# Performance work log

Hardware: AMD Instinct MI355X
Metric: run time of the kernel (lower is better)

The kernel has to match this reference:

```python
import jax, jax.numpy as jnp
import numpy as np


def setup_inputs() -> dict:
    key = jax.random.key(0)
    ks = jax.random.split(key, 8)
    T, D = 8192, 36
    return {
        "embeddings": jax.random.normal(ks[0], (T, D), dtype=jnp.float32),
        "WQ_prog": jax.random.normal(ks[1], (2, D), dtype=jnp.float32),
        "WK_prog": jax.random.normal(ks[2], (2, D), dtype=jnp.float32),
        "WV_op": jax.random.normal(ks[3], (1, D), dtype=jnp.float32),
        "WV_arg": jax.random.normal(ks[4], (1, D), dtype=jnp.float32),
        "WQ_stack": jax.random.normal(ks[5], (2, D), dtype=jnp.float32),
        "WK_stack": jax.random.normal(ks[6], (2, D), dtype=jnp.float32),
        "WV_stack": jax.random.normal(ks[7], (1, D), dtype=jnp.float32),
    }


def reference(embeddings, WQ_prog, WK_prog, WV_op, WV_arg, WQ_stack, WK_stack, WV_stack):
    # --- program-fetch head: hard-argmax attention ---
    Q_prog = embeddings @ WQ_prog.T          # (T, 2)
    K_prog = embeddings @ WK_prog.T          # (T, 2)
    V_op = embeddings @ WV_op.T              # (T, 1)
    V_arg = embeddings @ WV_arg.T            # (T, 1)
    scores_prog = Q_prog @ K_prog.T          # (T, T)
    best_prog = jnp.argmax(scores_prog, axis=1)   # (T,)
    fetched_ops = V_op[best_prog, 0]
    fetched_args = V_arg[best_prog, 0]

    # --- stack-fetch head: hard-argmax attention ---
    Q_stack = embeddings @ WQ_stack.T        # (T, 2)
    K_stack = embeddings @ WK_stack.T        # (T, 2)
    V_stack = embeddings @ WV_stack.T        # (T, 1)
    scores_stack = Q_stack @ K_stack.T       # (T, T)
    best_stack = jnp.argmax(scores_stack, axis=1)
    fetched_vals = V_stack[best_stack, 0]

    return (fetched_ops, fetched_args, fetched_vals)
```

## Files before the change

### kernel.cpp

```cpp
#include <hip/hip_runtime.h>
#include <math.h>

#define T 8192
#define D 36
#define NCH 64
#define CHUNK (T / NCH)
#define RPT 4


__global__ __launch_bounds__(256) void proj_kernel(
    const float* __restrict__ E,
    const float* __restrict__ WQp, const float* __restrict__ WKp,
    const float* __restrict__ WVop, const float* __restrict__ WVarg,
    const float* __restrict__ WQs, const float* __restrict__ WKs,
    const float* __restrict__ WVs, float* __restrict__ ws) {
    int t = blockIdx.x * blockDim.x + threadIdx.x;
    if (t >= T) return;
    float e[D];
    const float4* Er = (const float4*)(E + t * D);
#pragma unroll
    for (int i = 0; i < D / 4; ++i) {
        float4 v = Er[i];
        e[4 * i + 0] = v.x; e[4 * i + 1] = v.y;
        e[4 * i + 2] = v.z; e[4 * i + 3] = v.w;
    }
    float qp0 = 0.f, qp1 = 0.f, kp0 = 0.f, kp1 = 0.f;
    float qs0 = 0.f, qs1 = 0.f, ks0 = 0.f, ks1 = 0.f;
    float vop = 0.f, varg = 0.f, vs = 0.f;
#pragma unroll
    for (int d = 0; d < D; ++d) {
        float ed = e[d];
        qp0 = fmaf(ed, WQp[d], qp0);
        qp1 = fmaf(ed, WQp[D + d], qp1);
        kp0 = fmaf(ed, WKp[d], kp0);
        kp1 = fmaf(ed, WKp[D + d], kp1);
        qs0 = fmaf(ed, WQs[d], qs0);
        qs1 = fmaf(ed, WQs[D + d], qs1);
        ks0 = fmaf(ed, WKs[d], ks0);
        ks1 = fmaf(ed, WKs[D + d], ks1);
        vop  = fmaf(ed, WVop[d], vop);
        varg = fmaf(ed, WVarg[d], varg);
        vs   = fmaf(ed, WVs[d], vs);
    }
    float2* Qp = (float2*)ws;
    float2* Kp = (float2*)(ws + 2 * T);
    float2* Qs = (float2*)(ws + 4 * T);
    float2* Ks = (float2*)(ws + 6 * T);
    Qp[t] = make_float2(qp0, qp1);
    Kp[t] = make_float2(kp0, kp1);
    Qs[t] = make_float2(qs0, qs1);
    Ks[t] = make_float2(ks0, ks1);
    ws[8 * T + t]  = vop;
    ws[9 * T + t]  = varg;
    ws[10 * T + t] = vs;
}

__global__ __launch_bounds__(256) void argmax_kernel(
    const float* __restrict__ wsf, float2* __restrict__ part) {
    const int head = blockIdx.z;
    const float2* Q = (const float2*)(wsf + head * 4 * T);
    const float2* K = (const float2*)(wsf + 2 * T + head * 4 * T);

    __shared__ float2 sk[CHUNK];
    const int c  = blockIdx.y;
    const int j0 = c * CHUNK;
    if (threadIdx.x < CHUNK) sk[threadIdx.x] = K[j0 + threadIdx.x];
    __syncthreads();

    const int rbase = blockIdx.x * (256 * RPT) + threadIdx.x;
    float2 q[RPT];
    float best[RPT];
    int   bi[RPT];
#pragma unroll
    for (int i = 0; i < RPT; ++i) {
        q[i] = Q[rbase + 256 * i];
        best[i] = -INFINITY;
        bi[i] = 0;
    }
#pragma unroll 8
    for (int k = 0; k < CHUNK; ++k) {
        float2 kk = sk[k];
#pragma unroll
        for (int i = 0; i < RPT; ++i) {
            float s = fmaf(q[i].x, kk.x, q[i].y * kk.y);
            bool gt = s > best[i];
            best[i] = gt ? s : best[i];
            bi[i]   = gt ? k : bi[i];
        }
    }
#pragma unroll
    for (int i = 0; i < RPT; ++i) {
        const int prow = head * T + rbase + 256 * i;
        part[c * (2 * T) + prow] = make_float2(best[i], __int_as_float(j0 + bi[i]));
    }
}

__global__ __launch_bounds__(256) void finalize_kernel(
    const float* __restrict__ wsf, const float2* __restrict__ part,
    float* __restrict__ out) {
    int idx = blockIdx.x * blockDim.x + threadIdx.x;
    if (idx >= 2 * T) return;
    float best = -INFINITY;
    int bj = 0;
#pragma unroll
    for (int c = 0; c < NCH; ++c) {
        float2 p = part[c * (2 * T) + idx];
        bool gt = p.x > best;
        best = gt ? p.x : best;
        bj   = gt ? __float_as_int(p.y) : bj;
    }
    const int head = idx >> 13;
    const int row  = idx & (T - 1);
    const float* Vop  = wsf + 8 * T;
    const float* Varg = wsf + 9 * T;
    const float* Vs   = wsf + 10 * T;
    if (head == 0) {
        out[row]     = Vop[bj];
        out[T + row] = Varg[bj];
    } else {
        out[2 * T + row] = Vs[bj];
    }
}

extern "C" void kernel_launch(void* const* d_in, const int* in_sizes, int n_in,
                              void* d_out, int out_size, void* d_ws, size_t ws_size,
                              hipStream_t stream) {
    const float* E     = (const float*)d_in[0];
    const float* WQp   = (const float*)d_in[1];
    const float* WKp   = (const float*)d_in[2];
    const float* WVop  = (const float*)d_in[3];
    const float* WVarg = (const float*)d_in[4];
    const float* WQs   = (const float*)d_in[5];
    const float* WKs   = (const float*)d_in[6];
    const float* WVs   = (const float*)d_in[7];
    float* out = (float*)d_out;

    float* wsf = (float*)d_ws;
    float2* part = (float2*)(wsf + 11 * T);

    proj_kernel<<<T / 256, 256, 0, stream>>>(E, WQp, WKp, WVop, WVarg, WQs, WKs, WVs, wsf);

    dim3 gB(T / (256 * RPT), NCH, 2);
    argmax_kernel<<<gB, 256, 0, stream>>>(wsf, part);

    finalize_kernel<<<(2 * T) / 256, 256, 0, stream>>>(wsf, part, out);
}
```

Before: 110.8 us.

## Fuse projections into argmax kernel, split scan into even/odd chains

Drops the separate projection kernel. Each argmax block now computes its own K chunk and Q rows straight from the embeddings, and the finalize kernel recomputes the value projection only for the selected row. The key chunk grows from 128 to 256 (NCH from 64 to 32) so that each of the 256 threads computes one key. The inner scan keeps separate even and odd best trackers to break the serial compare dependency, and resolves ties to the lower index. This removes a kernel launch and the workspace round trip, at the cost of recomputing Q projections in every chunk block.

```diff
diff --git a/kernel.cpp b/kernel.cpp
--- a/kernel.cpp
+++ b/kernel.cpp
@@ -3,103 +3,98 @@
 
 #define T 8192
 #define D 36
-#define NCH 64
+#define NCH 32
 #define CHUNK (T / NCH)
 #define RPT 4
+#define RBLK (T / (256 * RPT))
 
 
-__global__ __launch_bounds__(256) void proj_kernel(
-    const float* __restrict__ E,
-    const float* __restrict__ WQp, const float* __restrict__ WKp,
-    const float* __restrict__ WVop, const float* __restrict__ WVarg,
-    const float* __restrict__ WQs, const float* __restrict__ WKs,
-    const float* __restrict__ WVs, float* __restrict__ ws) {
-    int t = blockIdx.x * blockDim.x + threadIdx.x;
-    if (t >= T) return;
-    float e[D];
-    const float4* Er = (const float4*)(E + t * D);
+__device__ __forceinline__ void dot2_row(const float* __restrict__ E, int row,
+                                         const float* __restrict__ W,
+                                         float& d0, float& d1) {
+    const float4* Er = (const float4*)(E + row * D);
+    float a0 = 0.f, a1 = 0.f;
 #pragma unroll
     for (int i = 0; i < D / 4; ++i) {
         float4 v = Er[i];
-        e[4 * i + 0] = v.x; e[4 * i + 1] = v.y;
-        e[4 * i + 2] = v.z; e[4 * i + 3] = v.w;
+        a0 = fmaf(v.x, W[4 * i + 0], a0);
+        a0 = fmaf(v.y, W[4 * i + 1], a0);
+        a0 = fmaf(v.z, W[4 * i + 2], a0);
+        a0 = fmaf(v.w, W[4 * i + 3], a0);
+        a1 = fmaf(v.x, W[D + 4 * i + 0], a1);
+        a1 = fmaf(v.y, W[D + 4 * i + 1], a1);
+        a1 = fmaf(v.z, W[D + 4 * i + 2], a1);
+        a1 = fmaf(v.w, W[D + 4 * i + 3], a1);
     }
-    float qp0 = 0.f, qp1 = 0.f, kp0 = 0.f, kp1 = 0.f;
-    float qs0 = 0.f, qs1 = 0.f, ks0 = 0.f, ks1 = 0.f;
-    float vop = 0.f, varg = 0.f, vs = 0.f;
-#pragma unroll
-    for (int d = 0; d < D; ++d) {
-        float ed = e[d];
-        qp0 = fmaf(ed, WQp[d], qp0);
-        qp1 = fmaf(ed, WQp[D + d], qp1);
-        kp0 = fmaf(ed, WKp[d], kp0);
-        kp1 = fmaf(ed, WKp[D + d], kp1);
-        qs0 = fmaf(ed, WQs[d], qs0);
-        qs1 = fmaf(ed, WQs[D + d], qs1);
-        ks0 = fmaf(ed, WKs[d], ks0);
-        ks1 = fmaf(ed, WKs[D + d], ks1);
-        vop  = fmaf(ed, WVop[d], vop);
-        varg = fmaf(ed, WVarg[d], varg);
-        vs   = fmaf(ed, WVs[d], vs);
-    }
-    float2* Qp = (float2*)ws;
-    float2* Kp = (float2*)(ws + 2 * T);
-    float2* Qs = (float2*)(ws + 4 * T);
-    float2* Ks = (float2*)(ws + 6 * T);
-    Qp[t] = make_float2(qp0, qp1);
-    Kp[t] = make_float2(kp0, kp1);
-    Qs[t] = make_float2(qs0, qs1);
-    Ks[t] = make_float2(ks0, ks1);
-    ws[8 * T + t]  = vop;
-    ws[9 * T + t]  = varg;
-    ws[10 * T + t] = vs;
+    d0 = a0; d1 = a1;
 }
 
-__global__ __launch_bounds__(256) void argmax_kernel(
-    const float* __restrict__ wsf, float2* __restrict__ part) {
+__global__ __launch_bounds__(256, 2) void fused_kernel(
+    const float* __restrict__ E,
+    const float* __restrict__ WQp, const float* __restrict__ WKp,
+    const float* __restrict__ WQs, const float* __restrict__ WKs,
+    float2* __restrict__ part) {
     const int head = blockIdx.z;
-    const float2* Q = (const float2*)(wsf + head * 4 * T);
-    const float2* K = (const float2*)(wsf + 2 * T + head * 4 * T);
+    const float* WQ = head ? WQs : WQp;
+    const float* WK = head ? WKs : WKp;
 
     __shared__ float2 sk[CHUNK];
-    const int c  = blockIdx.y;
-    const int j0 = c * CHUNK;
-    if (threadIdx.x < CHUNK) sk[threadIdx.x] = K[j0 + threadIdx.x];
+    const int j0 = blockIdx.y * CHUNK;
+
+    {
+        float k0, k1;
+        dot2_row(E, j0 + (int)threadIdx.x, WK, k0, k1);
+        sk[threadIdx.x] = make_float2(k0, k1);
+    }
+
+    const int rbase = blockIdx.x * (256 * RPT) + threadIdx.x;
+    float q0[RPT], q1[RPT];
+#pragma unroll
+    for (int i = 0; i < RPT; ++i)
+        dot2_row(E, rbase + 256 * i, WQ, q0[i], q1[i]);
+
     __syncthreads();
 
-    const int rbase = blockIdx.x * (256 * RPT) + threadIdx.x;
-    float2 q[RPT];
-    float best[RPT];
-    int   bi[RPT];
+    float beste[RPT], besto[RPT];
+    int bie[RPT], bio[RPT];
 #pragma unroll
     for (int i = 0; i < RPT; ++i) {
-        q[i] = Q[rbase + 256 * i];
-        best[i] = -INFINITY;
-        bi[i] = 0;
+        beste[i] = -INFINITY; besto[i] = -INFINITY;
+        bie[i] = 0; bio[i] = 1;
     }
-#pragma unroll 8
-    for (int k = 0; k < CHUNK; ++k) {
-        float2 kk = sk[k];
+#pragma unroll 4
+    for (int k = 0; k < CHUNK; k += 2) {
+        float2 ke = sk[k];
+        float2 ko = sk[k + 1];
 #pragma unroll
         for (int i = 0; i < RPT; ++i) {
-            float s = fmaf(q[i].x, kk.x, q[i].y * kk.y);
-            bool gt = s > best[i];
-            best[i] = gt ? s : best[i];
-            bi[i]   = gt ? k : bi[i];
+            float se = fmaf(q0[i], ke.x, q1[i] * ke.y);
+            float so = fmaf(q0[i], ko.x, q1[i] * ko.y);
+            bool ge = se > beste[i];
+            beste[i] = ge ? se : beste[i];
+            bie[i]   = ge ? k : bie[i];
+            bool go = so > besto[i];
+            besto[i] = go ? so : besto[i];
+            bio[i]   = go ? (k + 1) : bio[i];
         }
     }
 #pragma unroll
     for (int i = 0; i < RPT; ++i) {
+        bool ogt = besto[i] > beste[i];
+        float bv = ogt ? besto[i] : beste[i];
+        int bj   = ogt ? bio[i] : bie[i];
+        if (beste[i] == besto[i]) bj = min(bie[i], bio[i]);
         const int prow = head * T + rbase + 256 * i;
-        part[c * (2 * T) + prow] = make_float2(best[i], __int_as_float(j0 + bi[i]));
+        part[blockIdx.y * (2 * T) + prow] = make_float2(bv, __int_as_float(j0 + bj));
     }
 }
 
 __global__ __launch_bounds__(256) void finalize_kernel(
-    const float* __restrict__ wsf, const float2* __restrict__ part,
-    float* __restrict__ out) {
-    int idx = blockIdx.x * blockDim.x + threadIdx.x;
-    if (idx >= 2 * T) return;
+    const float* __restrict__ E,
+    const float* __restrict__ WVop, const float* __restrict__ WVarg,
+    const float* __restrict__ WVs,
+    const float2* __restrict__ part, float* __restrict__ out) {
+    int idx = blockIdx.x * 256 + threadIdx.x;
     float best = -INFINITY;
     int bj = 0;
 #pragma unroll
@@ -111,14 +106,28 @@
     }
     const int head = idx >> 13;
     const int row  = idx & (T - 1);
-    const float* Vop  = wsf + 8 * T;
-    const float* Varg = wsf + 9 * T;
-    const float* Vs   = wsf + 10 * T;
+    const float4* Er = (const float4*)(E + bj * D);
+    float e[D];
+#pragma unroll
+    for (int i = 0; i < D / 4; ++i) {
+        float4 v = Er[i];
+        e[4 * i + 0] = v.x; e[4 * i + 1] = v.y;
+        e[4 * i + 2] = v.z; e[4 * i + 3] = v.w;
+    }
     if (head == 0) {
-        out[row]     = Vop[bj];
-        out[T + row] = Varg[bj];
+        float vop = 0.f, varg = 0.f;
+#pragma unroll
+        for (int d = 0; d < D; ++d) {
+            vop  = fmaf(e[d], WVop[d], vop);
+            varg = fmaf(e[d], WVarg[d], varg);
+        }
+        out[row]     = vop;
+        out[T + row] = varg;
     } else {
-        out[2 * T + row] = Vs[bj];
+        float vs = 0.f;
+#pragma unroll
+        for (int d = 0; d < D; ++d) vs = fmaf(e[d], WVs[d], vs);
+        out[2 * T + row] = vs;
     }
 }
 
@@ -135,13 +144,10 @@
     const float* WVs   = (const float*)d_in[7];
     float* out = (float*)d_out;
 
-    float* wsf = (float*)d_ws;
-    float2* part = (float2*)(wsf + 11 * T);
+    float2* part = (float2*)d_ws;
 
-    proj_kernel<<<T / 256, 256, 0, stream>>>(E, WQp, WKp, WVop, WVarg, WQs, WKs, WVs, wsf);
+    dim3 gF(RBLK, NCH, 2);
+    fused_kernel<<<gF, 256, 0, stream>>>(E, WQp, WKp, WQs, WKs, part);
 
-    dim3 gB(T / (256 * RPT), NCH, 2);
-    argmax_kernel<<<gB, 256, 0, stream>>>(wsf, part);
-
-    finalize_kernel<<<(2 * T) / 256, 256, 0, stream>>>(wsf, part, out);
+    finalize_kernel<<<(2 * T) / 256, 256, 0, stream>>>(E, WVop, WVarg, WVs, part, out);
 }
```

Result: no change. 111.0 us (+0.1%).
